# Performance work log

Measured on AMD Instinct MI355X. Metric: run time of the kernel, lower is better.

Reference implementation:

```python
import jax, jax.numpy as jnp
import numpy as np

N_NODES = 100000
N_EDGES = 1600000
MOTIF_DIM = 32
HIDDEN = 64


def setup_inputs() -> dict:
    key = jax.random.key(0)
    k1, k2, k3, k4 = jax.random.split(key, 4)
    motif_x = jax.random.normal(k1, (N_NODES, MOTIF_DIM), dtype=jnp.float32)
    edge_index = jax.random.randint(k2, (2, N_EDGES), 0, N_NODES, dtype=jnp.int64)
    in_dim = 4 * MOTIF_DIM
    W1 = jax.random.normal(k3, (in_dim, HIDDEN), dtype=jnp.float32) / np.sqrt(in_dim)
    b1 = jnp.zeros((HIDDEN,), dtype=jnp.float32)
    W2 = jax.random.normal(k4, (HIDDEN, 1), dtype=jnp.float32) / np.sqrt(HIDDEN)
    b2 = jnp.zeros((1,), dtype=jnp.float32)
    return {"motif_x": motif_x, "edge_index": edge_index, "W1": W1, "b1": b1, "W2": W2, "b2": b2}


def reference(motif_x, edge_index, W1, b1, W2, b2):
    src = edge_index[0]
    dst = edge_index[1]
    mu = motif_x[src]                      # [E, D] gather
    mv = motif_x[dst]                      # [E, D] gather
    feats = jnp.concatenate([mu, mv, jnp.abs(mu - mv), mu * mv], axis=1)  # [E, 4D]
    h = jax.nn.relu(feats @ W1 + b1)       # [E, H]
    g = jax.nn.sigmoid(h @ W2 + b2)[:, 0]  # [E]
    return jnp.clip(g, 0.0, 1.0)
```

## Files before the change

### kernel.cpp

```cpp
#include <hip/hip_runtime.h>
#include <hip/hip_fp16.h>

#define D 32
#define H 64

typedef __attribute__((ext_vector_type(8))) _Float16 f16x8;
typedef __attribute__((ext_vector_type(4))) float f32x4;

union AB { uint4 u; f16x8 v; __half2 h2[4]; };

template <int CTRL>
__device__ __forceinline__ float dppadd(float x) {
  int s = __builtin_amdgcn_update_dpp(0, __float_as_int(x), CTRL, 0xF, 0xF, true);
  return x + __int_as_float(s);
}
__device__ __forceinline__ float row16_sum(float x) {
  x = dppadd<0xB1>(x);
  x = dppadd<0x4E>(x);
  x = dppadd<0x141>(x);
  x = dppadd<0x140>(x);
  return x;
}

__global__ __launch_bounds__(256) void prep(
    const float* __restrict__ x, const float* __restrict__ W1,
    unsigned short* __restrict__ xh, unsigned short* __restrict__ btab,
    int n4, int nPack) {
  int b = blockIdx.x;
  if (b < nPack) {
    int i = b * 256 + threadIdx.x;
    if (i < n4) {
      float4 v = ((const float4*)x)[i];
      ushort4 o;
      o.x = __half_as_ushort(__float2half(v.x));
      o.y = __half_as_ushort(__float2half(v.y));
      o.z = __half_as_ushort(__float2half(v.z));
      o.w = __half_as_ushort(__float2half(v.w));
      ((ushort4*)xh)[i] = o;
    }
  } else {
    int id = (b - nPack) * 256 + threadIdx.x;
    if (id < 16 * 64 * 8) {
      int j = id & 7;
      int l = (id >> 3) & 63;
      int f = id >> 9;
      int s = f & 3, t = f >> 2;
      int k = s * 32 + (l >> 4) * 8 + j;
      int n = t * 16 + (l & 15);
      btab[id] = __half_as_ushort(__float2half(W1[k * H + n]));
    }
  }
}

__device__ __forceinline__ void compute_pair(
    uint4 mu0U, uint4 mv0U, uint4 mu1U, uint4 mv1U,
    const _Float16* __restrict__ bl,
    const float* __restrict__ b1v, const float* __restrict__ w2v, float bias2,
    int pair, int q, int m, int nE, float* __restrict__ out) {
  AB mu0, mv0, mu1, mv1, ac0, ap0, ac1, ap1;
  mu0.u = mu0U; mv0.u = mv0U; mu1.u = mu1U; mv1.u = mv1U;
#pragma unroll
  for (int k = 0; k < 4; ++k) {
    ac0.h2[k] = __habs2(__hsub2(mu0.h2[k], mv0.h2[k]));
    ap0.h2[k] = __hmul2(mu0.h2[k], mv0.h2[k]);
    ac1.h2[k] = __habs2(__hsub2(mu1.h2[k], mv1.h2[k]));
    ap1.h2[k] = __hmul2(mu1.h2[k], mv1.h2[k]);
  }

  float part0[4], part1[4];
#pragma unroll
  for (int t = 0; t < 4; ++t) {
    float bv = b1v[t];
    f32x4 acc0 = (f32x4){bv, bv, bv, bv};
    f32x4 acc1 = (f32x4){bv, bv, bv, bv};
    f16x8 B0 = *(const f16x8*)(bl + (t * 4 + 0) * 512);
    acc0 = __builtin_amdgcn_mfma_f32_16x16x32_f16(mu0.v, B0, acc0, 0, 0, 0);
    acc1 = __builtin_amdgcn_mfma_f32_16x16x32_f16(mu1.v, B0, acc1, 0, 0, 0);
    f16x8 B1 = *(const f16x8*)(bl + (t * 4 + 1) * 512);
    acc0 = __builtin_amdgcn_mfma_f32_16x16x32_f16(mv0.v, B1, acc0, 0, 0, 0);
    acc1 = __builtin_amdgcn_mfma_f32_16x16x32_f16(mv1.v, B1, acc1, 0, 0, 0);
    f16x8 B2 = *(const f16x8*)(bl + (t * 4 + 2) * 512);
    acc0 = __builtin_amdgcn_mfma_f32_16x16x32_f16(ac0.v, B2, acc0, 0, 0, 0);
    acc1 = __builtin_amdgcn_mfma_f32_16x16x32_f16(ac1.v, B2, acc1, 0, 0, 0);
    f16x8 B3 = *(const f16x8*)(bl + (t * 4 + 3) * 512);
    acc0 = __builtin_amdgcn_mfma_f32_16x16x32_f16(ap0.v, B3, acc0, 0, 0, 0);
    acc1 = __builtin_amdgcn_mfma_f32_16x16x32_f16(ap1.v, B3, acc1, 0, 0, 0);
#pragma unroll
    for (int r = 0; r < 4; ++r) {
      float h0 = fmaxf(acc0[r], 0.f);
      float h1 = fmaxf(acc1[r], 0.f);
      part0[r] = (t == 0) ? h0 * w2v[0] : fmaf(h0, w2v[t], part0[r]);
      part1[r] = (t == 0) ? h1 * w2v[0] : fmaf(h1, w2v[t], part1[r]);
    }
  }

#pragma unroll
  for (int r = 0; r < 4; ++r) {
    part0[r] = row16_sum(part0[r]);
    part1[r] = row16_sum(part1[r]);
  }

  if (m < 4) {
    float z0 = (m == 0 ? part0[0] : m == 1 ? part0[1] : m == 2 ? part0[2] : part0[3]) + bias2;
    float z1 = (m == 0 ? part1[0] : m == 1 ? part1[1] : m == 2 ? part1[2] : part1[3]) + bias2;
    int ew0 = pair * 32 + q * 4 + m;
    int ew1 = pair * 32 + 16 + q * 4 + m;
    if (ew0 < nE) out[ew0] = 1.f / (1.f + __expf(-z0));
    if (ew1 < nE) out[ew1] = 1.f / (1.f + __expf(-z1));
  }
}

__global__ __launch_bounds__(256) void edge_mfma(
    const unsigned short* __restrict__ xh, const unsigned short* __restrict__ btab,
    const int* __restrict__ ei,
    const float* __restrict__ b1, const float* __restrict__ W2,
    const float* __restrict__ b2, float* __restrict__ out,
    int nE, int nPairs) {
  __shared__ _Float16 lds_b[16 * 64 * 8];

  {
    const uint4* src = (const uint4*)btab;
    uint4* dst = (uint4*)lds_b;
#pragma unroll
    for (int i = 0; i < 4; ++i)
      dst[threadIdx.x + i * 256] = src[threadIdx.x + i * 256];
  }
  __syncthreads();

  int lane = threadIdx.x & 63;
  int wid  = (blockIdx.x * 256 + threadIdx.x) >> 6;
  int nW   = (gridDim.x * 256) >> 6;
  int m = lane & 15;
  int q = lane >> 4;
  if (wid >= nPairs) return;

  float b1v[4], w2v[4];
#pragma unroll
  for (int t = 0; t < 4; ++t) {
    b1v[t] = b1[t * 16 + m];
    w2v[t] = W2[t * 16 + m];
  }
  float bias2 = b2[0];

  const uint4* xb = (const uint4*)xh;
  int eLim = nE - 1;
  int pLim = nPairs - 1;
  int selOff = (lane >> 5) ? nE : 0;
  int eoff = lane & 31;

  int p = wid;
  int idxNxt;
  uint4 amu0, amv0, amu1, amv1;
  {
    int e = p * 32 + eoff; e = e < nE ? e : eLim;
    int idxCur = ei[selOff + e];
    int sn0 = __shfl(idxCur, m);
    int sn1 = __shfl(idxCur, 16 + m);
    int dn0 = __shfl(idxCur, 32 + m);
    int dn1 = __shfl(idxCur, 48 + m);
    amu0 = xb[sn0 * 4 + q]; amv0 = xb[dn0 * 4 + q];
    amu1 = xb[sn1 * 4 + q]; amv1 = xb[dn1 * 4 + q];
    int p1 = p + nW; p1 = p1 < nPairs ? p1 : pLim;
    int e1 = p1 * 32 + eoff; e1 = e1 < nE ? e1 : eLim;
    idxNxt = ei[selOff + e1];
  }

  while (p < nPairs) {
    int pn = p + nW;
    int sn0 = __shfl(idxNxt, m);
    int sn1 = __shfl(idxNxt, 16 + m);
    int dn0 = __shfl(idxNxt, 32 + m);
    int dn1 = __shfl(idxNxt, 48 + m);
    uint4 bmu0 = xb[sn0 * 4 + q], bmv0 = xb[dn0 * 4 + q];
    uint4 bmu1 = xb[sn1 * 4 + q], bmv1 = xb[dn1 * 4 + q];
    {
      int p2 = pn + nW; p2 = p2 < nPairs ? p2 : pLim;
      int e2 = p2 * 32 + eoff; e2 = e2 < nE ? e2 : eLim;
      idxNxt = ei[selOff + e2];
    }

    int bofs = lane * 8;
    asm volatile("" : "+v"(bofs));
    const _Float16* bl = lds_b + bofs;

    compute_pair(amu0, amv0, amu1, amv1, bl, b1v, w2v, bias2, p, q, m, nE, out);

    amu0 = bmu0; amv0 = bmv0; amu1 = bmu1; amv1 = bmv1;
    p = pn;
  }
}

__global__ __launch_bounds__(256) void edge_full(
    const float* __restrict__ x, const int* __restrict__ ei,
    const float* __restrict__ W1, const float* __restrict__ b1,
    const float* __restrict__ W2, const float* __restrict__ b2,
    float* __restrict__ out, int nE) {
  int e = blockIdx.x * 256 + threadIdx.x;
  if (e >= nE) return;
  int s = ei[e];
  int d = ei[e + nE];
  const float4* mu4 = (const float4*)(x + (size_t)s * D);
  const float4* mv4 = (const float4*)(x + (size_t)d * D);
  float mu[D], mv[D], c[D], p[D];
#pragma unroll
  for (int qq = 0; qq < D / 4; ++qq) {
    float4 a = mu4[qq];
    float4 b = mv4[qq];
    mu[4*qq+0] = a.x; mv[4*qq+0] = b.x; c[4*qq+0] = fabsf(a.x-b.x); p[4*qq+0] = a.x*b.x;
    mu[4*qq+1] = a.y; mv[4*qq+1] = b.y; c[4*qq+1] = fabsf(a.y-b.y); p[4*qq+1] = a.y*b.y;
    mu[4*qq+2] = a.z; mv[4*qq+2] = b.z; c[4*qq+2] = fabsf(a.z-b.z); p[4*qq+2] = a.z*b.z;
    mu[4*qq+3] = a.w; mv[4*qq+3] = b.w; c[4*qq+3] = fabsf(a.w-b.w); p[4*qq+3] = a.w*b.w;
  }
  float z = b2[0];
  for (int j = 0; j < H; ++j) {
    float a = b1[j];
#pragma unroll
    for (int k = 0; k < D; ++k) {
      a = fmaf(mu[k], W1[k * H + j], a);
      a = fmaf(mv[k], W1[(D + k) * H + j], a);
      a = fmaf(c[k],  W1[(2 * D + k) * H + j], a);
      a = fmaf(p[k],  W1[(3 * D + k) * H + j], a);
    }
    a = fmaxf(a, 0.f);
    z = fmaf(a, W2[j], z);
  }
  float g = 1.f / (1.f + __expf(-z));
  out[e] = fminf(fmaxf(g, 0.f), 1.f);
}

extern "C" void kernel_launch(void* const* d_in, const int* in_sizes, int n_in,
                              void* d_out, int out_size, void* d_ws, size_t ws_size,
                              hipStream_t stream) {
  const float* x  = (const float*)d_in[0];
  const int*   ei = (const int*)d_in[1];
  const float* W1 = (const float*)d_in[2];
  const float* b1 = (const float*)d_in[3];
  const float* W2 = (const float*)d_in[4];
  const float* b2 = (const float*)d_in[5];
  float* out = (float*)d_out;

  int nN = in_sizes[0] / D;
  int nE = in_sizes[1] / 2;

  size_t xh_shorts = (size_t)nN * D;
  size_t need = (xh_shorts + 16 * 64 * 8) * sizeof(unsigned short);
  if (ws_size >= need) {
    unsigned short* xh   = (unsigned short*)d_ws;
    unsigned short* btab = xh + xh_shorts;
    int n4 = nN * D / 4;
    int nPack = (n4 + 255) / 256;
    int nBt = (16 * 64 * 8 + 255) / 256;
    prep<<<nPack + nBt, 256, 0, stream>>>(x, W1, xh, btab, n4, nPack);
    int nTiles = (nE + 15) / 16;
    int nPairs = (nTiles + 1) / 2;
    edge_mfma<<<2048, 256, 0, stream>>>(xh, btab, ei, b1, W2, b2, out, nE, nPairs);
  } else {
    edge_full<<<(nE + 255) / 256, 256, 0, stream>>>(x, ei, W1, b1, W2, b2, out, nE);
  }
}
```

Measured before the change: 118.1 us.

## Process four 16-edge tiles per wave iteration instead of two

Each wave now handles 64 edges per loop iteration, loading source and destination indices directly per lane and gathering four tiles of node features. Each LDS-loaded W1 fragment feeds four MFMAs instead of two, which amortizes LDS reads and loop overhead and keeps more gathers in flight for prefetch. The cost is higher register pressure from eight prefetched uint4s plus sixteen accumulators, which may reduce occupancy. With 2048 blocks the grid also covers groups in fewer iterations.

```diff
diff --git a/kernel.cpp b/kernel.cpp
--- a/kernel.cpp
+++ b/kernel.cpp
@@ -52,70 +52,12 @@
   }
 }
 
-__device__ __forceinline__ void compute_pair(
-    uint4 mu0U, uint4 mv0U, uint4 mu1U, uint4 mv1U,
-    const _Float16* __restrict__ bl,
-    const float* __restrict__ b1v, const float* __restrict__ w2v, float bias2,
-    int pair, int q, int m, int nE, float* __restrict__ out) {
-  AB mu0, mv0, mu1, mv1, ac0, ap0, ac1, ap1;
-  mu0.u = mu0U; mv0.u = mv0U; mu1.u = mu1U; mv1.u = mv1U;
-#pragma unroll
-  for (int k = 0; k < 4; ++k) {
-    ac0.h2[k] = __habs2(__hsub2(mu0.h2[k], mv0.h2[k]));
-    ap0.h2[k] = __hmul2(mu0.h2[k], mv0.h2[k]);
-    ac1.h2[k] = __habs2(__hsub2(mu1.h2[k], mv1.h2[k]));
-    ap1.h2[k] = __hmul2(mu1.h2[k], mv1.h2[k]);
-  }
-
-  float part0[4], part1[4];
-#pragma unroll
-  for (int t = 0; t < 4; ++t) {
-    float bv = b1v[t];
-    f32x4 acc0 = (f32x4){bv, bv, bv, bv};
-    f32x4 acc1 = (f32x4){bv, bv, bv, bv};
-    f16x8 B0 = *(const f16x8*)(bl + (t * 4 + 0) * 512);
-    acc0 = __builtin_amdgcn_mfma_f32_16x16x32_f16(mu0.v, B0, acc0, 0, 0, 0);
-    acc1 = __builtin_amdgcn_mfma_f32_16x16x32_f16(mu1.v, B0, acc1, 0, 0, 0);
-    f16x8 B1 = *(const f16x8*)(bl + (t * 4 + 1) * 512);
-    acc0 = __builtin_amdgcn_mfma_f32_16x16x32_f16(mv0.v, B1, acc0, 0, 0, 0);
-    acc1 = __builtin_amdgcn_mfma_f32_16x16x32_f16(mv1.v, B1, acc1, 0, 0, 0);
-    f16x8 B2 = *(const f16x8*)(bl + (t * 4 + 2) * 512);
-    acc0 = __builtin_amdgcn_mfma_f32_16x16x32_f16(ac0.v, B2, acc0, 0, 0, 0);
-    acc1 = __builtin_amdgcn_mfma_f32_16x16x32_f16(ac1.v, B2, acc1, 0, 0, 0);
-    f16x8 B3 = *(const f16x8*)(bl + (t * 4 + 3) * 512);
-    acc0 = __builtin_amdgcn_mfma_f32_16x16x32_f16(ap0.v, B3, acc0, 0, 0, 0);
-    acc1 = __builtin_amdgcn_mfma_f32_16x16x32_f16(ap1.v, B3, acc1, 0, 0, 0);
-#pragma unroll
-    for (int r = 0; r < 4; ++r) {
-      float h0 = fmaxf(acc0[r], 0.f);
-      float h1 = fmaxf(acc1[r], 0.f);
-      part0[r] = (t == 0) ? h0 * w2v[0] : fmaf(h0, w2v[t], part0[r]);
-      part1[r] = (t == 0) ? h1 * w2v[0] : fmaf(h1, w2v[t], part1[r]);
-    }
-  }
-
-#pragma unroll
-  for (int r = 0; r < 4; ++r) {
-    part0[r] = row16_sum(part0[r]);
-    part1[r] = row16_sum(part1[r]);
-  }
-
-  if (m < 4) {
-    float z0 = (m == 0 ? part0[0] : m == 1 ? part0[1] : m == 2 ? part0[2] : part0[3]) + bias2;
-    float z1 = (m == 0 ? part1[0] : m == 1 ? part1[1] : m == 2 ? part1[2] : part1[3]) + bias2;
-    int ew0 = pair * 32 + q * 4 + m;
-    int ew1 = pair * 32 + 16 + q * 4 + m;
-    if (ew0 < nE) out[ew0] = 1.f / (1.f + __expf(-z0));
-    if (ew1 < nE) out[ew1] = 1.f / (1.f + __expf(-z1));
-  }
-}
-
 __global__ __launch_bounds__(256) void edge_mfma(
     const unsigned short* __restrict__ xh, const unsigned short* __restrict__ btab,
     const int* __restrict__ ei,
     const float* __restrict__ b1, const float* __restrict__ W2,
     const float* __restrict__ b2, float* __restrict__ out,
-    int nE, int nPairs) {
+    int nE, int nGroups) {
   __shared__ _Float16 lds_b[16 * 64 * 8];
 
   {
@@ -132,7 +74,7 @@
   int nW   = (gridDim.x * 256) >> 6;
   int m = lane & 15;
   int q = lane >> 4;
-  if (wid >= nPairs) return;
+  if (wid >= nGroups) return;
 
   float b1v[4], w2v[4];
 #pragma unroll
@@ -144,49 +86,125 @@
 
   const uint4* xb = (const uint4*)xh;
   int eLim = nE - 1;
-  int pLim = nPairs - 1;
-  int selOff = (lane >> 5) ? nE : 0;
-  int eoff = lane & 31;
-
-  int p = wid;
-  int idxNxt;
-  uint4 amu0, amv0, amu1, amv1;
+  int gLim = nGroups - 1;
+
+  int g = wid;
+  int idxS, idxD;
+  uint4 amu[4], amv[4];
   {
-    int e = p * 32 + eoff; e = e < nE ? e : eLim;
-    int idxCur = ei[selOff + e];
-    int sn0 = __shfl(idxCur, m);
-    int sn1 = __shfl(idxCur, 16 + m);
-    int dn0 = __shfl(idxCur, 32 + m);
-    int dn1 = __shfl(idxCur, 48 + m);
-    amu0 = xb[sn0 * 4 + q]; amv0 = xb[dn0 * 4 + q];
-    amu1 = xb[sn1 * 4 + q]; amv1 = xb[dn1 * 4 + q];
-    int p1 = p + nW; p1 = p1 < nPairs ? p1 : pLim;
-    int e1 = p1 * 32 + eoff; e1 = e1 < nE ? e1 : eLim;
-    idxNxt = ei[selOff + e1];
-  }
-
-  while (p < nPairs) {
-    int pn = p + nW;
-    int sn0 = __shfl(idxNxt, m);
-    int sn1 = __shfl(idxNxt, 16 + m);
-    int dn0 = __shfl(idxNxt, 32 + m);
-    int dn1 = __shfl(idxNxt, 48 + m);
-    uint4 bmu0 = xb[sn0 * 4 + q], bmv0 = xb[dn0 * 4 + q];
-    uint4 bmu1 = xb[sn1 * 4 + q], bmv1 = xb[dn1 * 4 + q];
+    int e0 = g * 64 + lane; e0 = e0 < nE ? e0 : eLim;
+    idxS = ei[e0]; idxD = ei[e0 + nE];
+#pragma unroll
+    for (int t = 0; t < 4; ++t) {
+      int sn = __shfl(idxS, t * 16 + m);
+      int dn = __shfl(idxD, t * 16 + m);
+      amu[t] = xb[sn * 4 + q];
+      amv[t] = xb[dn * 4 + q];
+    }
+    int g1 = g + nW; g1 = g1 < nGroups ? g1 : gLim;
+    int e1 = g1 * 64 + lane; e1 = e1 < nE ? e1 : eLim;
+    idxS = ei[e1]; idxD = ei[e1 + nE];
+  }
+
+#pragma unroll 2
+  for (; g < nGroups; ) {
+    int gn = g + nW;
+    uint4 bmu[4], bmv[4];
+#pragma unroll
+    for (int t = 0; t < 4; ++t) {
+      int sn = __shfl(idxS, t * 16 + m);
+      int dn = __shfl(idxD, t * 16 + m);
+      bmu[t] = xb[sn * 4 + q];
+      bmv[t] = xb[dn * 4 + q];
+    }
     {
-      int p2 = pn + nW; p2 = p2 < nPairs ? p2 : pLim;
-      int e2 = p2 * 32 + eoff; e2 = e2 < nE ? e2 : eLim;
-      idxNxt = ei[selOff + e2];
+      int g2 = gn + nW; g2 = g2 < nGroups ? g2 : gLim;
+      int e2 = g2 * 64 + lane; e2 = e2 < nE ? e2 : eLim;
+      idxS = ei[e2]; idxD = ei[e2 + nE];
+    }
+
+    AB mu[4], mv[4], ac[4], ap[4];
+#pragma unroll
+    for (int ti = 0; ti < 4; ++ti) {
+      mu[ti].u = amu[ti]; mv[ti].u = amv[ti];
+#pragma unroll
+      for (int k = 0; k < 4; ++k) {
+        ac[ti].h2[k] = __habs2(__hsub2(mu[ti].h2[k], mv[ti].h2[k]));
+        ap[ti].h2[k] = __hmul2(mu[ti].h2[k], mv[ti].h2[k]);
+      }
     }
 
     int bofs = lane * 8;
     asm volatile("" : "+v"(bofs));
     const _Float16* bl = lds_b + bofs;
 
-    compute_pair(amu0, amv0, amu1, amv1, bl, b1v, w2v, bias2, p, q, m, nE, out);
-
-    amu0 = bmu0; amv0 = bmv0; amu1 = bmu1; amv1 = bmv1;
-    p = pn;
+    float part[4][4];
+#pragma unroll
+    for (int t = 0; t < 4; ++t) {
+      float bv = b1v[t];
+      f32x4 acc0 = (f32x4){bv, bv, bv, bv};
+      f32x4 acc1 = (f32x4){bv, bv, bv, bv};
+      f32x4 acc2 = (f32x4){bv, bv, bv, bv};
+      f32x4 acc3 = (f32x4){bv, bv, bv, bv};
+      f16x8 B0 = *(const f16x8*)(bl + (t * 4 + 0) * 512);
+      acc0 = __builtin_amdgcn_mfma_f32_16x16x32_f16(mu[0].v, B0, acc0, 0, 0, 0);
+      acc1 = __builtin_amdgcn_mfma_f32_16x16x32_f16(mu[1].v, B0, acc1, 0, 0, 0);
+      acc2 = __builtin_amdgcn_mfma_f32_16x16x32_f16(mu[2].v, B0, acc2, 0, 0, 0);
+      acc3 = __builtin_amdgcn_mfma_f32_16x16x32_f16(mu[3].v, B0, acc3, 0, 0, 0);
+      f16x8 B1 = *(const f16x8*)(bl + (t * 4 + 1) * 512);
+      acc0 = __builtin_amdgcn_mfma_f32_16x16x32_f16(mv[0].v, B1, acc0, 0, 0, 0);
+      acc1 = __builtin_amdgcn_mfma_f32_16x16x32_f16(mv[1].v, B1, acc1, 0, 0, 0);
+      acc2 = __builtin_amdgcn_mfma_f32_16x16x32_f16(mv[2].v, B1, acc2, 0, 0, 0);
+      acc3 = __builtin_amdgcn_mfma_f32_16x16x32_f16(mv[3].v, B1, acc3, 0, 0, 0);
+      f16x8 B2 = *(const f16x8*)(bl + (t * 4 + 2) * 512);
+      acc0 = __builtin_amdgcn_mfma_f32_16x16x32_f16(ac[0].v, B2, acc0, 0, 0, 0);
+      acc1 = __builtin_amdgcn_mfma_f32_16x16x32_f16(ac[1].v, B2, acc1, 0, 0, 0);
+      acc2 = __builtin_amdgcn_mfma_f32_16x16x32_f16(ac[2].v, B2, acc2, 0, 0, 0);
+      acc3 = __builtin_amdgcn_mfma_f32_16x16x32_f16(ac[3].v, B2, acc3, 0, 0, 0);
+      f16x8 B3 = *(const f16x8*)(bl + (t * 4 + 3) * 512);
+      acc0 = __builtin_amdgcn_mfma_f32_16x16x32_f16(ap[0].v, B3, acc0, 0, 0, 0);
+      acc1 = __builtin_amdgcn_mfma_f32_16x16x32_f16(ap[1].v, B3, acc1, 0, 0, 0);
+      acc2 = __builtin_amdgcn_mfma_f32_16x16x32_f16(ap[2].v, B3, acc2, 0, 0, 0);
+      acc3 = __builtin_amdgcn_mfma_f32_16x16x32_f16(ap[3].v, B3, acc3, 0, 0, 0);
+#pragma unroll
+      for (int r = 0; r < 4; ++r) {
+        float h0 = fmaxf(acc0[r], 0.f);
+        float h1 = fmaxf(acc1[r], 0.f);
+        float h2 = fmaxf(acc2[r], 0.f);
+        float h3 = fmaxf(acc3[r], 0.f);
+        if (t == 0) {
+          part[0][r] = h0 * w2v[0]; part[1][r] = h1 * w2v[0];
+          part[2][r] = h2 * w2v[0]; part[3][r] = h3 * w2v[0];
+        } else {
+          part[0][r] = fmaf(h0, w2v[t], part[0][r]);
+          part[1][r] = fmaf(h1, w2v[t], part[1][r]);
+          part[2][r] = fmaf(h2, w2v[t], part[2][r]);
+          part[3][r] = fmaf(h3, w2v[t], part[3][r]);
+        }
+      }
+    }
+
+#pragma unroll
+    for (int ti = 0; ti < 4; ++ti)
+#pragma unroll
+      for (int r = 0; r < 4; ++r)
+        part[ti][r] = row16_sum(part[ti][r]);
+
+    if (m < 4) {
+#pragma unroll
+      for (int ti = 0; ti < 4; ++ti) {
+        int ew = g * 64 + ti * 16 + q * 4 + m;
+        if (ew < nE) {
+          float z = (m == 0 ? part[ti][0] : m == 1 ? part[ti][1]
+                     : m == 2 ? part[ti][2] : part[ti][3]) + bias2;
+          out[ew] = 1.f / (1.f + __expf(-z));
+        }
+      }
+    }
+
+#pragma unroll
+    for (int t = 0; t < 4; ++t) { amu[t] = bmu[t]; amv[t] = bmv[t]; }
+    g = gn;
   }
 }
 
@@ -251,9 +269,8 @@
     int nPack = (n4 + 255) / 256;
     int nBt = (16 * 64 * 8 + 255) / 256;
     prep<<<nPack + nBt, 256, 0, stream>>>(x, W1, xh, btab, n4, nPack);
-    int nTiles = (nE + 15) / 16;
-    int nPairs = (nTiles + 1) / 2;
-    edge_mfma<<<2048, 256, 0, stream>>>(xh, btab, ei, b1, W2, b2, out, nE, nPairs);
+    int nGroups = (nE + 63) / 64;
+    edge_mfma<<<2048, 256, 0, stream>>>(xh, btab, ei, b1, W2, b2, out, nE, nGroups);
   } else {
     edge_full<<<(nE + 255) / 256, 256, 0, stream>>>(x, ei, W1, b1, W2, b2, out, nE);
   }
```

Measured after the change: 128.9 us. 9.1% more time.
